# Performance work log

Hardware: AMD Instinct MI355X
Metric: run time of the kernel (lower is better)

The kernel has to match this reference:

```python
import jax, jax.numpy as jnp
import numpy as np

EMB = 512
HEADS = 8
HEAD_DIM = EMB // HEADS


def setup_inputs() -> dict:
    key = jax.random.key(0)
    ks = jax.random.split(key, 9)
    s = 1.0 / np.sqrt(EMB)
    return {
        "x": jax.random.normal(ks[0], (4, 2048, EMB), dtype=jnp.float32),
        "Wq": jax.random.uniform(ks[1], (EMB, EMB), jnp.float32, -s, s),
        "bq": jax.random.uniform(ks[2], (EMB,), jnp.float32, -s, s),
        "Wk": jax.random.uniform(ks[3], (EMB, EMB), jnp.float32, -s, s),
        "bk": jax.random.uniform(ks[4], (EMB,), jnp.float32, -s, s),
        "Wv": jax.random.uniform(ks[5], (EMB, EMB), jnp.float32, -s, s),
        "bv": jax.random.uniform(ks[6], (EMB,), jnp.float32, -s, s),
        "Wp": jax.random.uniform(ks[7], (EMB, EMB), jnp.float32, -s, s),
        "bp": jax.random.uniform(ks[8], (EMB,), jnp.float32, -s, s),
    }


def _split_heads(t):
    b, n, _ = t.shape
    return t.reshape(b, n, HEADS, HEAD_DIM).transpose(0, 2, 1, 3)  # b h n d


def reference(x, Wq, bq, Wk, bk, Wv, bv, Wp, bp):
    q = _split_heads(x @ Wq.T + bq)
    k = _split_heads(x @ Wk.T + bk)
    v = _split_heads(x @ Wv.T + bv)
    energy = jnp.einsum("bhqd,bhkd->bhqk", q, k)
    # NOTE: original applies softmax to UNSCALED logits, then divides probs by sqrt(emb)
    att = jax.nn.softmax(energy, axis=-1) / jnp.sqrt(jnp.float32(EMB))
    out = jnp.einsum("bhqk,bhkd->bhqd", att, v)
    b, h, n, d = out.shape
    out = out.transpose(0, 2, 1, 3).reshape(b, n, h * d)
    return out @ Wp.T + bp
```

## Files before the change

kernel.cpp:

```cpp
#include <hip/hip_runtime.h>
#include <math.h>
#include <stdint.h>

#define SEQ  2048
#define NH   8
#define HD   64
#define MTOT 8192
#define LOG2E 1.4426950408889634f

typedef __attribute__((ext_vector_type(4))) float f32x4;
typedef __attribute__((ext_vector_type(16))) float f32x16;
typedef __attribute__((ext_vector_type(8))) short bf16x8;

template <int V> struct IC { static constexpr int value = V; };

__device__ __forceinline__ unsigned packbf(float a, float b) {
    return __builtin_amdgcn_perm(__float_as_uint(b) + 0x8000u,
                                 __float_as_uint(a) + 0x8000u, 0x07060302u);
}

__device__ __forceinline__ void gl_lds16(const void* g, const void* l) {
    __builtin_amdgcn_global_load_lds(
        (const __attribute__((address_space(1))) unsigned int*)g,
        (__attribute__((address_space(3))) unsigned int*)l, 16, 0, 0);
}

__global__ __launch_bounds__(256) void convert_kernel(
    const float* __restrict__ x,  const float* __restrict__ wq,
    const float* __restrict__ wk, const float* __restrict__ wv,
    const float* __restrict__ wp, unsigned short* __restrict__ dst)
{
    const long i = ((long)blockIdx.x * 256 + threadIdx.x) * 4;
    if (i >= 5242880L) return;
    const float* src; long off;
    if      (i < 4194304L) { src = x;  off = i; }
    else if (i < 4456448L) { src = wq; off = i - 4194304L; }
    else if (i < 4718592L) { src = wk; off = i - 4456448L; }
    else if (i < 4980736L) { src = wv; off = i - 4718592L; }
    else                   { src = wp; off = i - 4980736L; }
    const float4 a = *(const float4*)(src + off);
    uint2 o;
    o.x = packbf(a.x, a.y);
    o.y = packbf(a.z, a.w);
    *(uint2*)(dst + i) = o;
}

template <int MODE>
__global__ __launch_bounds__(256, MODE == 0 ? 3 : 2) void gemm_kernel(
    const unsigned short* __restrict__ A, const unsigned short* __restrict__ W,
    const float* __restrict__ b0, const float* __restrict__ b1,
    const float* __restrict__ b2,
    unsigned short* __restrict__ Qw, unsigned short* __restrict__ Kw,
    unsigned short* __restrict__ VTw, float* __restrict__ Fout)
{
    constexpr int BN = (MODE == 0) ? 128 : 64;
    constexpr int NT = BN / 32;
    constexpr int BSTR = BN * 32;
    __shared__ __align__(16) unsigned short smem[16384];
    const int t = threadIdx.x;
    const int w = t >> 6, lane = t & 63, quad = (t >> 4) & 3, l15 = t & 15;
    const int wr = w >> 1, wc = w & 1;
    const int m0 = blockIdx.y * 128;
    const int n0 = blockIdx.x * BN;

    f32x4 acc[4][NT];
#pragma unroll
    for (int mt = 0; mt < 4; ++mt)
#pragma unroll
        for (int nt = 0; nt < NT; ++nt) acc[mt][nt] = (f32x4){0.f, 0.f, 0.f, 0.f};

    auto stage = [&](int buf, int k0) {
#pragma unroll
        for (int i = 0; i < 2; ++i) {
            const int ci = w * 2 + i;
            gl_lds16(A + (size_t)(m0 + ci * 16 + l15) * 512 + k0 + quad * 8,
                     smem + buf * 4096 + ci * 512);
            if (MODE == 0)
                gl_lds16(W + (size_t)(n0 + ci * 16 + l15) * 512 + k0 + quad * 8,
                         smem + 8192 + buf * BSTR + ci * 512);
        }
        if (MODE == 1)
            gl_lds16(W + (size_t)(n0 + w * 16 + l15) * 512 + k0 + quad * 8,
                     smem + 8192 + buf * BSTR + w * 512);
    };

    int buf = 0;
    stage(0, 0);
    __syncthreads();

    auto kloop = [&](auto TRC) {
        constexpr int TR = decltype(TRC)::value;
        for (int ki = 0; ki < 16; ++ki) {
            if (ki < 15) stage(buf ^ 1, (ki + 1) * 32);
            const unsigned short* As = smem + buf * 4096;
            const unsigned short* Bs = smem + 8192 + buf * BSTR;
            bf16x8 af[4], bfr[NT];
#pragma unroll
            for (int mt = 0; mt < 4; ++mt)
                af[mt] = *(const bf16x8*)(As + ((wr * 4 + mt) * 64 + lane) * 8);
#pragma unroll
            for (int nt = 0; nt < NT; ++nt)
                bfr[nt] = *(const bf16x8*)(Bs + ((wc * NT + nt) * 64 + lane) * 8);
#pragma unroll
            for (int mt = 0; mt < 4; ++mt)
#pragma unroll
                for (int nt = 0; nt < NT; ++nt) {
                    if (TR)
                        acc[mt][nt] = __builtin_amdgcn_mfma_f32_16x16x32_bf16(
                            bfr[nt], af[mt], acc[mt][nt], 0, 0, 0);
                    else
                        acc[mt][nt] = __builtin_amdgcn_mfma_f32_16x16x32_bf16(
                            af[mt], bfr[nt], acc[mt][nt], 0, 0, 0);
                }
            buf ^= 1;
            if (ki < 15) __syncthreads();
        }
    };
    if (MODE == 0 && n0 < 1024) kloop(IC<1>{});
    else                        kloop(IC<0>{});

    if (MODE == 1) {
#pragma unroll
        for (int nt = 0; nt < NT; ++nt) {
            const int n = n0 + wc * 32 + nt * 16 + l15;
            const float bias = b0[n];
#pragma unroll
            for (int mt = 0; mt < 4; ++mt) {
                const int mb = m0 + wr * 64 + mt * 16 + quad * 4;
                const f32x4 v = acc[mt][nt];
#pragma unroll
                for (int r = 0; r < 4; ++r)
                    Fout[(size_t)(mb + r) * 512 + n] = v[r] + bias;
            }
        }
    } else if (n0 >= 1024) {
#pragma unroll
        for (int nt = 0; nt < 4; ++nt) {
            const int n = n0 + wc * 64 + nt * 16 + l15;
            const float bias = b2[n & 511];
            const int h = (n >> 6) & 7, d = n & 63;
#pragma unroll
            for (int mt = 0; mt < 4; ++mt) {
                const int mb = m0 + wr * 64 + mt * 16 + quad * 4;
                const int bi = mb >> 11, ns = mb & 2047;
                const int bhl = bi * 8 + h;
                const f32x4 v = acc[mt][nt];
                uint2 pk;
                pk.x = packbf(v[0] + bias, v[1] + bias);
                pk.y = packbf(v[2] + bias, v[3] + bias);
                const size_t off =
                    ((size_t)(bhl * 32 + (ns >> 6)) * 8 + ((d >> 5) << 2) +
                     ((ns >> 4) & 3)) * 512 +
                    ((d & 31) << 3) + ((ns & 8) << 5) + (ns & 7);
                *(uint2*)(VTw + off) = pk;
            }
        }
    } else {
        const int which = n0 >> 9;
        const float sc = which ? 1.f : LOG2E;
        const float* bp = which ? b1 : b0;
        unsigned short* base = which ? Kw : Qw;
#pragma unroll
        for (int nt = 0; nt < 4; ++nt) {
            const int nb = n0 + wc * 64 + nt * 16 + quad * 4;
            const f32x4 bv = *(const f32x4*)(bp + (nb & 511));
            const int h = (nb >> 6) & 7, d0 = nb & 63;
#pragma unroll
            for (int mt = 0; mt < 4; ++mt) {
                const int nsg = m0 + wr * 64 + mt * 16 + l15;
                const int bi = nsg >> 11, ns = nsg & 2047;
                const int bhl = bi * 8 + h;
                const f32x4 v = acc[mt][nt];
                uint2 pk;
                pk.x = packbf((v[0] + bv[0]) * sc, (v[1] + bv[1]) * sc);
                pk.y = packbf((v[2] + bv[2]) * sc, (v[3] + bv[3]) * sc);
                const size_t off =
                    ((size_t)(bhl * 64 + (ns >> 5)) * 4 + (d0 >> 4)) * 512 +
                    ((d0 & 8) << 5) + ((ns & 31) << 3) + (d0 & 7);
                *(uint2*)(base + off) = pk;
            }
        }
    }
}

__global__ __launch_bounds__(256, 2) void attn_kernel(
    const unsigned short* __restrict__ Qf, const unsigned short* __restrict__ Kf,
    const unsigned short* __restrict__ Vf, unsigned short* __restrict__ Ow)
{
    const int t = threadIdx.x;
    const int w = t >> 6, lane = t & 63;
    const int l31 = lane & 31, hlf = lane >> 5;

    const int bh = blockIdx.x;
    const int q0 = blockIdx.y * 128;
    const int qg = (q0 >> 5) + w;

    const unsigned short* Qp = Qf + ((size_t)(bh * 64 + qg) * 4) * 512 + lane * 8;
    const unsigned short* Kp = Kf + (size_t)bh * 131072 + lane * 8;
    const unsigned short* Vp = Vf + (size_t)bh * 131072 + lane * 8;

    bf16x8 qf[4];
#pragma unroll
    for (int kt = 0; kt < 4; ++kt)
        qf[kt] = *(const bf16x8*)(Qp + kt * 512);

    f32x16 zero;
#pragma unroll
    for (int r = 0; r < 16; ++r) zero[r] = 0.f;

    float lpart = 0.f;
    f32x16 Ot[2];
    Ot[0] = zero; Ot[1] = zero;

    bf16x8 kc[8];
#pragma unroll
    for (int c = 0; c < 8; ++c)
        kc[c] = *(const bf16x8*)(Kp + c * 512);

    for (int jt = 0; jt < 32; ++jt) {
        bf16x8 vc[8];
#pragma unroll
        for (int c = 0; c < 8; ++c)
            vc[c] = *(const bf16x8*)(Vp + jt * 4096 + c * 512);
        const int jn = (jt < 31) ? jt + 1 : 31;
        bf16x8 kn[8];
#pragma unroll
        for (int c = 0; c < 8; ++c)
            kn[c] = *(const bf16x8*)(Kp + jn * 4096 + c * 512);

        f32x16 st[2];
        st[0] = zero; st[1] = zero;
#pragma unroll
        for (int kt = 0; kt < 4; ++kt) {
            st[0] = __builtin_amdgcn_mfma_f32_32x32x16_bf16(kc[kt],     qf[kt], st[0], 0, 0, 0);
            st[1] = __builtin_amdgcn_mfma_f32_32x32x16_bf16(kc[4 + kt], qf[kt], st[1], 0, 0, 0);
        }

        float ls = 0.f;
#pragma unroll
        for (int jg = 0; jg < 2; ++jg)
#pragma unroll
            for (int r = 0; r < 16; ++r) {
                st[jg][r] = __builtin_amdgcn_exp2f(st[jg][r]);
                ls += st[jg][r];
            }
        lpart += ls;

        bf16x8 pf[4];
#pragma unroll
        for (int p = 0; p < 4; ++p) {
            const f32x16 c = st[p >> 1];
            const int r0 = (p & 1) * 8;
            const unsigned a0 = packbf(c[r0 + 0], c[r0 + 1]);
            const unsigned a1 = packbf(c[r0 + 2], c[r0 + 3]);
            const unsigned b0 = packbf(c[r0 + 4], c[r0 + 5]);
            const unsigned b1 = packbf(c[r0 + 6], c[r0 + 7]);
            const unsigned ta0 = (unsigned)__shfl_xor((int)a0, 32);
            const unsigned ta1 = (unsigned)__shfl_xor((int)a1, 32);
            const unsigned tb0 = (unsigned)__shfl_xor((int)b0, 32);
            const unsigned tb1 = (unsigned)__shfl_xor((int)b1, 32);
            union { unsigned u[4]; bf16x8 v; } pb;
            pb.u[0] = hlf ? tb0 : a0;
            pb.u[1] = hlf ? tb1 : a1;
            pb.u[2] = hlf ? b0 : ta0;
            pb.u[3] = hlf ? b1 : ta1;
            pf[p] = pb.v;
        }

#pragma unroll
        for (int dg = 0; dg < 2; ++dg)
#pragma unroll
            for (int p = 0; p < 4; ++p)
                Ot[dg] = __builtin_amdgcn_mfma_f32_32x32x16_bf16(
                    vc[dg * 4 + p], pf[p], Ot[dg], 0, 0, 0);

#pragma unroll
        for (int c = 0; c < 8; ++c) kc[c] = kn[c];
    }

    const float lv = lpart + __shfl_xor(lpart, 32);
    const float inv = 1.0f / (lv * 22.627416997969522f);

    const int bi = bh >> 3, h = bh & 7;
    const int ns = q0 + w * 32 + l31;
    unsigned short* dst = Ow + ((size_t)bi * SEQ + ns) * 512 + h * 64 + hlf * 4;
#pragma unroll
    for (int dg = 0; dg < 2; ++dg)
#pragma unroll
        for (int rb = 0; rb < 4; ++rb) {
            uint2 pk;
            pk.x = packbf(Ot[dg][rb * 4 + 0] * inv, Ot[dg][rb * 4 + 1] * inv);
            pk.y = packbf(Ot[dg][rb * 4 + 2] * inv, Ot[dg][rb * 4 + 3] * inv);
            *(uint2*)(dst + dg * 32 + rb * 8) = pk;
        }
}

extern "C" void kernel_launch(void* const* d_in, const int* in_sizes, int n_in,
                              void* d_out, int out_size, void* d_ws, size_t ws_size,
                              hipStream_t stream)
{
    const float* x  = (const float*)d_in[0];
    const float* Wq = (const float*)d_in[1];
    const float* bq = (const float*)d_in[2];
    const float* Wk = (const float*)d_in[3];
    const float* bk = (const float*)d_in[4];
    const float* Wv = (const float*)d_in[5];
    const float* bv = (const float*)d_in[6];
    const float* Wp = (const float*)d_in[7];
    const float* bp = (const float*)d_in[8];

    unsigned short* ws = (unsigned short*)d_ws;
    unsigned short* xb    = ws;
    unsigned short* Wqkvb = ws + 4194304;
    unsigned short* Wpb   = ws + 4980736;
    unsigned short* Qw    = ws + 5242880;
    unsigned short* Kw    = Qw + 4194304;
    unsigned short* VTw   = Kw + 4194304;
    unsigned short* Owb   = VTw + 4194304;

    convert_kernel<<<5120, 256, 0, stream>>>(x, Wq, Wk, Wv, Wp, ws);
    gemm_kernel<0><<<dim3(12, 64), 256, 0, stream>>>(
        xb, Wqkvb, bq, bk, bv, Qw, Kw, VTw, nullptr);
    attn_kernel<<<dim3(32, 16), 256, 0, stream>>>(Qw, Kw, VTw, Owb);
    gemm_kernel<1><<<dim3(8, 64), 256, 0, stream>>>(
        Owb, Wpb, bp, nullptr, nullptr, nullptr, nullptr, nullptr, (float*)d_out);
}
```

Before: 171.2 us.

## Fuse fp32-to-bf16 conversion into GEMMs and split attention keys across waves

The separate conversion kernel is removed. The QKV and output-projection GEMMs now load fp32 inputs and weights into registers, pack them to bf16 and store them to LDS, replacing the async global-to-LDS path and its double buffer. The attention kernel now uses 64-query tiles, with each pair of waves splitting the key range and combining partial outputs and row sums through LDS. This removes one launch and the bf16 workspace round trip and doubles the attention grid, at the cost of register-staged loads with less latency hiding and an extra LDS reduction in attention.

After: 169.6 us. About the same (-0.9%).

```diff
diff --git a/kernel.cpp b/kernel.cpp
--- a/kernel.cpp
+++ b/kernel.cpp
@@ -19,92 +19,85 @@
                                  __float_as_uint(a) + 0x8000u, 0x07060302u);
 }
 
-__device__ __forceinline__ void gl_lds16(const void* g, const void* l) {
-    __builtin_amdgcn_global_load_lds(
-        (const __attribute__((address_space(1))) unsigned int*)g,
-        (__attribute__((address_space(3))) unsigned int*)l, 16, 0, 0);
-}
-
-__global__ __launch_bounds__(256) void convert_kernel(
-    const float* __restrict__ x,  const float* __restrict__ wq,
-    const float* __restrict__ wk, const float* __restrict__ wv,
-    const float* __restrict__ wp, unsigned short* __restrict__ dst)
+__global__ __launch_bounds__(256, 3) void qkv_kernel(
+    const float* __restrict__ xf, const float* __restrict__ wqf,
+    const float* __restrict__ wkf, const float* __restrict__ wvf,
+    const float* __restrict__ bq, const float* __restrict__ bk,
+    const float* __restrict__ bv,
+    unsigned short* __restrict__ Qw, unsigned short* __restrict__ Kw,
+    unsigned short* __restrict__ VTw)
 {
-    const long i = ((long)blockIdx.x * 256 + threadIdx.x) * 4;
-    if (i >= 5242880L) return;
-    const float* src; long off;
-    if      (i < 4194304L) { src = x;  off = i; }
-    else if (i < 4456448L) { src = wq; off = i - 4194304L; }
-    else if (i < 4718592L) { src = wk; off = i - 4456448L; }
-    else if (i < 4980736L) { src = wv; off = i - 4718592L; }
-    else                   { src = wp; off = i - 4980736L; }
-    const float4 a = *(const float4*)(src + off);
-    uint2 o;
-    o.x = packbf(a.x, a.y);
-    o.y = packbf(a.z, a.w);
-    *(uint2*)(dst + i) = o;
-}
-
-template <int MODE>
-__global__ __launch_bounds__(256, MODE == 0 ? 3 : 2) void gemm_kernel(
-    const unsigned short* __restrict__ A, const unsigned short* __restrict__ W,
-    const float* __restrict__ b0, const float* __restrict__ b1,
-    const float* __restrict__ b2,
-    unsigned short* __restrict__ Qw, unsigned short* __restrict__ Kw,
-    unsigned short* __restrict__ VTw, float* __restrict__ Fout)
-{
-    constexpr int BN = (MODE == 0) ? 128 : 64;
-    constexpr int NT = BN / 32;
-    constexpr int BSTR = BN * 32;
-    __shared__ __align__(16) unsigned short smem[16384];
+    __shared__ __align__(16) unsigned short smem[8192];
+    unsigned short* As = smem;
+    unsigned short* Bs = smem + 4096;
+
     const int t = threadIdx.x;
     const int w = t >> 6, lane = t & 63, quad = (t >> 4) & 3, l15 = t & 15;
     const int wr = w >> 1, wc = w & 1;
     const int m0 = blockIdx.y * 128;
-    const int n0 = blockIdx.x * BN;
-
-    f32x4 acc[4][NT];
+    const int n0 = blockIdx.x * 128;
+    const int which = n0 >> 9;
+    const float* wbase = which == 0 ? wqf : (which == 1 ? wkf : wvf);
+    const int nrow = n0 & 511;
+
+    const int ar = t >> 2, akq = t & 3;
+    const float* ax = xf + (size_t)(m0 + ar) * 512 + akq * 8;
+    const float* bx = wbase + (size_t)(nrow + ar) * 512 + akq * 8;
+    const int lws = (ar & 15) | (akq << 4);
+    const int off0 = (ar >> 4) * 512 + lws * 8;
+    const int off1 = off0 + 4 * 512;
+
+    f32x4 acc[4][4];
 #pragma unroll
     for (int mt = 0; mt < 4; ++mt)
 #pragma unroll
-        for (int nt = 0; nt < NT; ++nt) acc[mt][nt] = (f32x4){0.f, 0.f, 0.f, 0.f};
-
-    auto stage = [&](int buf, int k0) {
-#pragma unroll
-        for (int i = 0; i < 2; ++i) {
-            const int ci = w * 2 + i;
-            gl_lds16(A + (size_t)(m0 + ci * 16 + l15) * 512 + k0 + quad * 8,
-                     smem + buf * 4096 + ci * 512);
-            if (MODE == 0)
-                gl_lds16(W + (size_t)(n0 + ci * 16 + l15) * 512 + k0 + quad * 8,
-                         smem + 8192 + buf * BSTR + ci * 512);
-        }
-        if (MODE == 1)
-            gl_lds16(W + (size_t)(n0 + w * 16 + l15) * 512 + k0 + quad * 8,
-                     smem + 8192 + buf * BSTR + w * 512);
+        for (int nt = 0; nt < 4; ++nt) acc[mt][nt] = (f32x4){0.f, 0.f, 0.f, 0.f};
+
+    float4 ra[4], rb[4];
+    auto loadt = [&](int k0) {
+        ra[0] = *(const float4*)(ax + k0);
+        ra[1] = *(const float4*)(ax + k0 + 4);
+        ra[2] = *(const float4*)(ax + 32768 + k0);
+        ra[3] = *(const float4*)(ax + 32768 + k0 + 4);
+        rb[0] = *(const float4*)(bx + k0);
+        rb[1] = *(const float4*)(bx + k0 + 4);
+        rb[2] = *(const float4*)(bx + 32768 + k0);
+        rb[3] = *(const float4*)(bx + 32768 + k0 + 4);
     };
-
-    int buf = 0;
-    stage(0, 0);
-    __syncthreads();
-
+    auto writet = [&]() {
+        uint4 p;
+        p.x = packbf(ra[0].x, ra[0].y); p.y = packbf(ra[0].z, ra[0].w);
+        p.z = packbf(ra[1].x, ra[1].y); p.w = packbf(ra[1].z, ra[1].w);
+        *(uint4*)(As + off0) = p;
+        p.x = packbf(ra[2].x, ra[2].y); p.y = packbf(ra[2].z, ra[2].w);
+        p.z = packbf(ra[3].x, ra[3].y); p.w = packbf(ra[3].z, ra[3].w);
+        *(uint4*)(As + off1) = p;
+        p.x = packbf(rb[0].x, rb[0].y); p.y = packbf(rb[0].z, rb[0].w);
+        p.z = packbf(rb[1].x, rb[1].y); p.w = packbf(rb[1].z, rb[1].w);
+        *(uint4*)(Bs + off0) = p;
+        p.x = packbf(rb[2].x, rb[2].y); p.y = packbf(rb[2].z, rb[2].w);
+        p.z = packbf(rb[3].x, rb[3].y); p.w = packbf(rb[3].z, rb[3].w);
+        *(uint4*)(Bs + off1) = p;
+    };
+
+    loadt(0);
     auto kloop = [&](auto TRC) {
         constexpr int TR = decltype(TRC)::value;
         for (int ki = 0; ki < 16; ++ki) {
-            if (ki < 15) stage(buf ^ 1, (ki + 1) * 32);
-            const unsigned short* As = smem + buf * 4096;
-            const unsigned short* Bs = smem + 8192 + buf * BSTR;
-            bf16x8 af[4], bfr[NT];
+            writet();
+            if (ki < 15) loadt((ki + 1) * 32);
+            __syncthreads();
+            bf16x8 af[4], bfr[4];
 #pragma unroll
             for (int mt = 0; mt < 4; ++mt)
                 af[mt] = *(const bf16x8*)(As + ((wr * 4 + mt) * 64 + lane) * 8);
 #pragma unroll
-            for (int nt = 0; nt < NT; ++nt)
-                bfr[nt] = *(const bf16x8*)(Bs + ((wc * NT + nt) * 64 + lane) * 8);
+            for (int nt = 0; nt < 4; ++nt)
+                bfr[nt] = *(const bf16x8*)(Bs + ((wc * 4 + nt) * 64 + lane) * 8);
 #pragma unroll
             for (int mt = 0; mt < 4; ++mt)
 #pragma unroll
-                for (int nt = 0; nt < NT; ++nt) {
+                for (int nt = 0; nt < 4; ++nt) {
                     if (TR)
                         acc[mt][nt] = __builtin_amdgcn_mfma_f32_16x16x32_bf16(
                             bfr[nt], af[mt], acc[mt][nt], 0, 0, 0);
@@ -112,32 +105,17 @@
                         acc[mt][nt] = __builtin_amdgcn_mfma_f32_16x16x32_bf16(
                             af[mt], bfr[nt], acc[mt][nt], 0, 0, 0);
                 }
-            buf ^= 1;
             if (ki < 15) __syncthreads();
         }
     };
-    if (MODE == 0 && n0 < 1024) kloop(IC<1>{});
-    else                        kloop(IC<0>{});
-
-    if (MODE == 1) {
-#pragma unroll
-        for (int nt = 0; nt < NT; ++nt) {
-            const int n = n0 + wc * 32 + nt * 16 + l15;
-            const float bias = b0[n];
-#pragma unroll
-            for (int mt = 0; mt < 4; ++mt) {
-                const int mb = m0 + wr * 64 + mt * 16 + quad * 4;
-                const f32x4 v = acc[mt][nt];
-#pragma unroll
-                for (int r = 0; r < 4; ++r)
-                    Fout[(size_t)(mb + r) * 512 + n] = v[r] + bias;
-            }
-        }
-    } else if (n0 >= 1024) {
+    if (which < 2) kloop(IC<1>{});
+    else           kloop(IC<0>{});
+
+    if (which == 2) {
 #pragma unroll
         for (int nt = 0; nt < 4; ++nt) {
             const int n = n0 + wc * 64 + nt * 16 + l15;
-            const float bias = b2[n & 511];
+            const float bias = bv[n & 511];
             const int h = (n >> 6) & 7, d = n & 63;
 #pragma unroll
             for (int mt = 0; mt < 4; ++mt) {
@@ -156,14 +134,13 @@
             }
         }
     } else {
-        const int which = n0 >> 9;
         const float sc = which ? 1.f : LOG2E;
-        const float* bp = which ? b1 : b0;
+        const float* bp = which ? bk : bq;
         unsigned short* base = which ? Kw : Qw;
 #pragma unroll
         for (int nt = 0; nt < 4; ++nt) {
             const int nb = n0 + wc * 64 + nt * 16 + quad * 4;
-            const f32x4 bv = *(const f32x4*)(bp + (nb & 511));
+            const f32x4 bvv = *(const f32x4*)(bp + (nb & 511));
             const int h = (nb >> 6) & 7, d0 = nb & 63;
 #pragma unroll
             for (int mt = 0; mt < 4; ++mt) {
@@ -172,8 +149,8 @@
                 const int bhl = bi * 8 + h;
                 const f32x4 v = acc[mt][nt];
                 uint2 pk;
-                pk.x = packbf((v[0] + bv[0]) * sc, (v[1] + bv[1]) * sc);
-                pk.y = packbf((v[2] + bv[2]) * sc, (v[3] + bv[3]) * sc);
+                pk.x = packbf((v[0] + bvv[0]) * sc, (v[1] + bvv[1]) * sc);
+                pk.y = packbf((v[2] + bvv[2]) * sc, (v[3] + bvv[3]) * sc);
                 const size_t off =
                     ((size_t)(bhl * 64 + (ns >> 5)) * 4 + (d0 >> 4)) * 512 +
                     ((d0 & 8) << 5) + ((ns & 31) << 3) + (d0 & 7);
@@ -183,20 +160,103 @@
     }
 }
 
-__global__ __launch_bounds__(256, 2) void attn_kernel(
+__global__ __launch_bounds__(256, 3) void outproj_kernel(
+    const unsigned short* __restrict__ Aw, const float* __restrict__ wpf,
+    const float* __restrict__ bp, float* __restrict__ out)
+{
+    __shared__ __align__(16) unsigned short smem[6144];
+    unsigned short* As = smem;
+    unsigned short* Bs = smem + 4096;
+
+    const int t = threadIdx.x;
+    const int w = t >> 6, lane = t & 63, quad = (t >> 4) & 3, l15 = t & 15;
+    const int wr = w >> 1, wc = w & 1;
+    const int m0 = blockIdx.y * 128;
+    const int n0 = blockIdx.x * 64;
+
+    const int ar = t >> 2, akq = t & 3;
+    const unsigned short* ap = Aw + (size_t)(m0 + ar) * 512 + akq * 8;
+    const float* bx = wpf + (size_t)(n0 + ar) * 512 + akq * 8;
+    const int lws = (ar & 15) | (akq << 4);
+    const int off0 = (ar >> 4) * 512 + lws * 8;
+    const int off1 = off0 + 4 * 512;
+    const int boff = (ar >> 4) * 512 + lws * 8;
+
+    f32x4 acc[4][2];
+#pragma unroll
+    for (int mt = 0; mt < 4; ++mt)
+#pragma unroll
+        for (int nt = 0; nt < 2; ++nt) acc[mt][nt] = (f32x4){0.f, 0.f, 0.f, 0.f};
+
+    uint4 ra0, ra1;
+    float4 rb0, rb1;
+    auto loadt = [&](int k0) {
+        ra0 = *(const uint4*)(ap + k0);
+        ra1 = *(const uint4*)(ap + 32768 + k0);
+        rb0 = *(const float4*)(bx + k0);
+        rb1 = *(const float4*)(bx + k0 + 4);
+    };
+    auto writet = [&]() {
+        *(uint4*)(As + off0) = ra0;
+        *(uint4*)(As + off1) = ra1;
+        uint4 p;
+        p.x = packbf(rb0.x, rb0.y); p.y = packbf(rb0.z, rb0.w);
+        p.z = packbf(rb1.x, rb1.y); p.w = packbf(rb1.z, rb1.w);
+        *(uint4*)(Bs + boff) = p;
+    };
+
+    loadt(0);
+    for (int ki = 0; ki < 16; ++ki) {
+        writet();
+        if (ki < 15) loadt((ki + 1) * 32);
+        __syncthreads();
+        bf16x8 af[4], bfr[2];
+#pragma unroll
+        for (int mt = 0; mt < 4; ++mt)
+            af[mt] = *(const bf16x8*)(As + ((wr * 4 + mt) * 64 + lane) * 8);
+#pragma unroll
+        for (int nt = 0; nt < 2; ++nt)
+            bfr[nt] = *(const bf16x8*)(Bs + ((wc * 2 + nt) * 64 + lane) * 8);
+#pragma unroll
+        for (int mt = 0; mt < 4; ++mt)
+#pragma unroll
+            for (int nt = 0; nt < 2; ++nt)
+                acc[mt][nt] = __builtin_amdgcn_mfma_f32_16x16x32_bf16(
+                    af[mt], bfr[nt], acc[mt][nt], 0, 0, 0);
+        if (ki < 15) __syncthreads();
+    }
+
+#pragma unroll
+    for (int nt = 0; nt < 2; ++nt) {
+        const int n = n0 + wc * 32 + nt * 16 + l15;
+        const float bias = bp[n];
+#pragma unroll
+        for (int mt = 0; mt < 4; ++mt) {
+            const int mb = m0 + wr * 64 + mt * 16 + quad * 4;
+            const f32x4 v = acc[mt][nt];
+#pragma unroll
+            for (int r = 0; r < 4; ++r)
+                out[(size_t)(mb + r) * 512 + n] = v[r] + bias;
+        }
+    }
+}
+
+__global__ __launch_bounds__(256, 4) void attn_kernel(
     const unsigned short* __restrict__ Qf, const unsigned short* __restrict__ Kf,
     const unsigned short* __restrict__ Vf, unsigned short* __restrict__ Ow)
 {
+    __shared__ float cb[4224];
     const int t = threadIdx.x;
     const int w = t >> 6, lane = t & 63;
     const int l31 = lane & 31, hlf = lane >> 5;
+    const int qh = w >> 1, jh = w & 1;
 
     const int bh = blockIdx.x;
-    const int q0 = blockIdx.y * 128;
-    const int qg = (q0 >> 5) + w;
+    const int q0 = blockIdx.y * 64;
+    const int qg = (q0 >> 5) + qh;
 
     const unsigned short* Qp = Qf + ((size_t)(bh * 64 + qg) * 4) * 512 + lane * 8;
-    const unsigned short* Kp = Kf + (size_t)bh * 131072 + lane * 8;
+    const unsigned short* Kp = Kf + (size_t)bh * 131072 + (jh * 4) * 512 + lane * 8;
     const unsigned short* Vp = Vf + (size_t)bh * 131072 + lane * 8;
 
     bf16x8 qf[4];
@@ -212,49 +272,46 @@
     f32x16 Ot[2];
     Ot[0] = zero; Ot[1] = zero;
 
-    bf16x8 kc[8];
-#pragma unroll
-    for (int c = 0; c < 8; ++c)
+    bf16x8 kc[4];
+#pragma unroll
+    for (int c = 0; c < 4; ++c)
         kc[c] = *(const bf16x8*)(Kp + c * 512);
 
     for (int jt = 0; jt < 32; ++jt) {
-        bf16x8 vc[8];
-#pragma unroll
-        for (int c = 0; c < 8; ++c)
-            vc[c] = *(const bf16x8*)(Vp + jt * 4096 + c * 512);
+        bf16x8 vc[4];
+#pragma unroll
+        for (int dg = 0; dg < 2; ++dg)
+#pragma unroll
+            for (int p = 0; p < 2; ++p)
+                vc[dg * 2 + p] = *(const bf16x8*)(
+                    Vp + (size_t)jt * 4096 + (dg * 4 + jh * 2 + p) * 512);
+
+        f32x16 st = zero;
+#pragma unroll
+        for (int kt = 0; kt < 4; ++kt)
+            st = __builtin_amdgcn_mfma_f32_32x32x16_bf16(kc[kt], qf[kt], st, 0, 0, 0);
+
         const int jn = (jt < 31) ? jt + 1 : 31;
-        bf16x8 kn[8];
-#pragma unroll
-        for (int c = 0; c < 8; ++c)
-            kn[c] = *(const bf16x8*)(Kp + jn * 4096 + c * 512);
-
-        f32x16 st[2];
-        st[0] = zero; st[1] = zero;
-#pragma unroll
-        for (int kt = 0; kt < 4; ++kt) {
-            st[0] = __builtin_amdgcn_mfma_f32_32x32x16_bf16(kc[kt],     qf[kt], st[0], 0, 0, 0);
-            st[1] = __builtin_amdgcn_mfma_f32_32x32x16_bf16(kc[4 + kt], qf[kt], st[1], 0, 0, 0);
-        }
+#pragma unroll
+        for (int c = 0; c < 4; ++c)
+            kc[c] = *(const bf16x8*)(Kp + (size_t)jn * 4096 + c * 512);
 
         float ls = 0.f;
 #pragma unroll
-        for (int jg = 0; jg < 2; ++jg)
-#pragma unroll
-            for (int r = 0; r < 16; ++r) {
-                st[jg][r] = __builtin_amdgcn_exp2f(st[jg][r]);
-                ls += st[jg][r];
-            }
+        for (int r = 0; r < 16; ++r) {
+            st[r] = __builtin_amdgcn_exp2f(st[r]);
+            ls += st[r];
+        }
         lpart += ls;
 
-        bf16x8 pf[4];
-#pragma unroll
-        for (int p = 0; p < 4; ++p) {
-            const f32x16 c = st[p >> 1];
-            const int r0 = (p & 1) * 8;
-            const unsigned a0 = packbf(c[r0 + 0], c[r0 + 1]);
-            const unsigned a1 = packbf(c[r0 + 2], c[r0 + 3]);
-            const unsigned b0 = packbf(c[r0 + 4], c[r0 + 5]);
-            const unsigned b1 = packbf(c[r0 + 6], c[r0 + 7]);
+        bf16x8 pf[2];
+#pragma unroll
+        for (int p = 0; p < 2; ++p) {
+            const int r0 = p * 8;
+            const unsigned a0 = packbf(st[r0 + 0], st[r0 + 1]);
+            const unsigned a1 = packbf(st[r0 + 2], st[r0 + 3]);
+            const unsigned b0 = packbf(st[r0 + 4], st[r0 + 5]);
+            const unsigned b1 = packbf(st[r0 + 6], st[r0 + 7]);
             const unsigned ta0 = (unsigned)__shfl_xor((int)a0, 32);
             const unsigned ta1 = (unsigned)__shfl_xor((int)a1, 32);
             const unsigned tb0 = (unsigned)__shfl_xor((int)b0, 32);
@@ -270,29 +327,50 @@
 #pragma unroll
         for (int dg = 0; dg < 2; ++dg)
 #pragma unroll
-            for (int p = 0; p < 4; ++p)
+            for (int p = 0; p < 2; ++p)
                 Ot[dg] = __builtin_amdgcn_mfma_f32_32x32x16_bf16(
-                    vc[dg * 4 + p], pf[p], Ot[dg], 0, 0, 0);
-
-#pragma unroll
-        for (int c = 0; c < 8; ++c) kc[c] = kn[c];
-    }
-
-    const float lv = lpart + __shfl_xor(lpart, 32);
-    const float inv = 1.0f / (lv * 22.627416997969522f);
-
-    const int bi = bh >> 3, h = bh & 7;
-    const int ns = q0 + w * 32 + l31;
-    unsigned short* dst = Ow + ((size_t)bi * SEQ + ns) * 512 + h * 64 + hlf * 4;
-#pragma unroll
-    for (int dg = 0; dg < 2; ++dg)
-#pragma unroll
-        for (int rb = 0; rb < 4; ++rb) {
-            uint2 pk;
-            pk.x = packbf(Ot[dg][rb * 4 + 0] * inv, Ot[dg][rb * 4 + 1] * inv);
-            pk.y = packbf(Ot[dg][rb * 4 + 2] * inv, Ot[dg][rb * 4 + 3] * inv);
-            *(uint2*)(dst + dg * 32 + rb * 8) = pk;
-        }
+                    vc[dg * 2 + p], pf[p], Ot[dg], 0, 0, 0);
+    }
+
+    if (jh == 1) {
+#pragma unroll
+        for (int dg = 0; dg < 2; ++dg)
+#pragma unroll
+            for (int k = 0; k < 4; ++k) {
+                float4 v = make_float4(Ot[dg][k * 4 + 0], Ot[dg][k * 4 + 1],
+                                       Ot[dg][k * 4 + 2], Ot[dg][k * 4 + 3]);
+                *(float4*)(cb + ((qh * 2 + dg) * 4 + k) * 256 + lane * 4) = v;
+            }
+        cb[4096 + qh * 64 + lane] = lpart;
+    }
+    __syncthreads();
+    if (jh == 0) {
+#pragma unroll
+        for (int dg = 0; dg < 2; ++dg)
+#pragma unroll
+            for (int k = 0; k < 4; ++k) {
+                const float4 v =
+                    *(const float4*)(cb + ((qh * 2 + dg) * 4 + k) * 256 + lane * 4);
+                Ot[dg][k * 4 + 0] += v.x; Ot[dg][k * 4 + 1] += v.y;
+                Ot[dg][k * 4 + 2] += v.z; Ot[dg][k * 4 + 3] += v.w;
+            }
+        float lv = lpart + cb[4096 + qh * 64 + lane];
+        lv += __shfl_xor(lv, 32);
+        const float inv = 1.0f / (lv * 22.627416997969522f);
+
+        const int bi = bh >> 3, h = bh & 7;
+        const int ns = q0 + qh * 32 + l31;
+        unsigned short* dst = Ow + ((size_t)bi * SEQ + ns) * 512 + h * 64 + hlf * 4;
+#pragma unroll
+        for (int dg = 0; dg < 2; ++dg)
+#pragma unroll
+            for (int rb = 0; rb < 4; ++rb) {
+                uint2 pk;
+                pk.x = packbf(Ot[dg][rb * 4 + 0] * inv, Ot[dg][rb * 4 + 1] * inv);
+                pk.y = packbf(Ot[dg][rb * 4 + 2] * inv, Ot[dg][rb * 4 + 3] * inv);
+                *(uint2*)(dst + dg * 32 + rb * 8) = pk;
+            }
+    }
 }
 
 extern "C" void kernel_launch(void* const* d_in, const int* in_sizes, int n_in,
@@ -310,18 +388,13 @@
     const float* bp = (const float*)d_in[8];
 
     unsigned short* ws = (unsigned short*)d_ws;
-    unsigned short* xb    = ws;
-    unsigned short* Wqkvb = ws + 4194304;
-    unsigned short* Wpb   = ws + 4980736;
-    unsigned short* Qw    = ws + 5242880;
-    unsigned short* Kw    = Qw + 4194304;
-    unsigned short* VTw   = Kw + 4194304;
-    unsigned short* Owb   = VTw + 4194304;
-
-    convert_kernel<<<5120, 256, 0, stream>>>(x, Wq, Wk, Wv, Wp, ws);
-    gemm_kernel<0><<<dim3(12, 64), 256, 0, stream>>>(
-        xb, Wqkvb, bq, bk, bv, Qw, Kw, VTw, nullptr);
-    attn_kernel<<<dim3(32, 16), 256, 0, stream>>>(Qw, Kw, VTw, Owb);
-    gemm_kernel<1><<<dim3(8, 64), 256, 0, stream>>>(
-        Owb, Wpb, bp, nullptr, nullptr, nullptr, nullptr, nullptr, (float*)d_out);
+    unsigned short* Qw  = ws;
+    unsigned short* Kw  = Qw + 4194304;
+    unsigned short* VTw = Kw + 4194304;
+    unsigned short* Owb = VTw + 4194304;
+
+    qkv_kernel<<<dim3(12, 64), 256, 0, stream>>>(
+        x, Wq, Wk, Wv, bq, bk, bv, Qw, Kw, VTw);
+    attn_kernel<<<dim3(32, 32), 256, 0, stream>>>(Qw, Kw, VTw, Owb);
+    outproj_kernel<<<dim3(8, 64), 256, 0, stream>>>(Owb, Wp, bp, (float*)d_out);
 }
```
